# Optimization experiments

Hardware: AMD Instinct MI355X
Metric: run time of the kernel (lower is better)

The kernel has to match this reference:

```python
import jax, jax.numpy as jnp
import numpy as np

NB, BS, NHID, NINP = 6, 200, 1200, 2400  # num_blocks, block_size, nhid, ninp (=2*nhid)
T, B, NTOK = 32, 32, 16000


def _ln(x, g, b):
    mu = x.mean(-1, keepdims=True)
    v = ((x - mu) ** 2).mean(-1, keepdims=True)
    return (x - mu) / jnp.sqrt(v + 1e-5) * g + b


def _attend(q3, k3, v3, wq, wk, wv, wfc, g, b, nh, dk, dv, residual):
    # q3/k3/v3: (B, L, d_model); multi-head scaled-dot attention across blocks
    Bz, L, _ = q3.shape
    qh = (q3 @ wq).reshape(Bz, L, nh, dk)
    kh = (k3 @ wk).reshape(Bz, L, nh, dk)
    vh = (v3 @ wv).reshape(Bz, L, nh, dv)
    att = jnp.einsum('bqhd,bkhd->bhqk', qh, kh) / float(np.sqrt(dk))
    att = jax.nn.softmax(att, axis=-1)
    out = jnp.einsum('bhqk,bkhd->bqhd', att, vh).reshape(Bz, L, nh * dv)
    out = out @ wfc
    if residual:
        out = out + q3
    return _ln(out, g, b)


def setup_inputs() -> dict:
    key = jax.random.key(0)
    ks = jax.random.split(key, 16)
    rn = lambda i, sh, s: jax.random.normal(ks[i], sh, dtype=jnp.float32) * s
    d = {}
    d['tokens'] = jax.random.randint(ks[0], (T, B), 0, NTOK)
    d['h0'] = jnp.zeros((2, B, NHID), jnp.float32)
    d['c0'] = jnp.zeros((2, B, NHID), jnp.float32)
    d['emb_table'] = jax.random.uniform(ks[1], (NTOK, NINP), jnp.float32, -0.1, 0.1)
    d['Wi'] = rn(2, (NB, 4 * BS, NINP), 0.01)
    d['Wh'] = rn(3, (NB, 4 * BS, BS), 0.05)
    d['bih'] = jnp.zeros((NB, 4 * BS), jnp.float32)
    d['bhh'] = jnp.zeros((NB, 4 * BS), jnp.float32)
    d['mq'] = rn(4, (BS, 64), 0.07)
    d['mk'] = rn(5, (BS, 64), 0.07)
    d['mv'] = rn(6, (BS, 64), 0.07)
    d['mfc'] = rn(7, (64, BS), 0.1)
    d['mg'] = jnp.ones((BS,), jnp.float32)
    d['mb'] = jnp.zeros((BS,), jnp.float32)
    d['lq'] = rn(8, (BS, 1600), 0.07)
    d['lk'] = rn(9, (BS, 1600), 0.07)
    d['lv'] = rn(10, (BS, 1600), 0.07)
    d['lfc'] = rn(11, (1600, 2400), 0.02)
    d['lg'] = jnp.ones((2400,), jnp.float32)
    d['lb'] = jnp.zeros((2400,), jnp.float32)
    d['dec_w'] = jax.random.uniform(ks[12], (NTOK, NHID), jnp.float32, -0.1, 0.1)
    d['dec_b'] = jnp.zeros((NTOK,), jnp.float32)
    return d


def reference(tokens, h0, c0, emb_table, Wi, Wh, bih, bhh, mq, mk, mv, mfc, mg, mb,
              lq, lk, lv, lfc, lg, lb, dec_w, dec_b):
    def block_lstm(x, h, c):
        # block-diagonal LSTMCell: k independent cells, per-block input NINP, hidden BS
        Bz = x.shape[0]
        xb = x.reshape(Bz, NB, -1)
        hb = h.reshape(Bz, NB, BS)
        cb = c.reshape(Bz, NB, BS)
        gt = jnp.einsum('bki,kgi->bkg', xb, Wi) + jnp.einsum('bkh,kgh->bkg', hb, Wh) + bih + bhh
        ii, ff, gg, oo = jnp.split(gt, 4, axis=-1)  # torch LSTMCell gate order i,f,g,o
        cn = jax.nn.sigmoid(ff) * cb + jax.nn.sigmoid(ii) * jnp.tanh(gg)
        hn = jax.nn.sigmoid(oo) * jnp.tanh(cn)
        return hn.reshape(Bz, NHID), cn.reshape(Bz, NHID)

    def self_att(h):
        hb = h.reshape(-1, NB, BS)
        hb = _attend(hb, hb, hb, mq, mk, mv, mfc, mg, mb, 4, 16, 16, True)
        return hb.reshape(-1, NHID)

    emb = emb_table[tokens]  # (T, B, NINP)

    def step0(carry, x):
        h, c = carry
        h, c = block_lstm(jnp.tile(x, (1, NB)), h, c)
        h = self_att(h)
        return (h, c), h

    (hf0, cf0), out = jax.lax.scan(step0, (h0[0], c0[0]), emb)

    def step1(carry, x):
        h, c = carry
        q = h.reshape(-1, NB, BS)
        kv = x.reshape(-1, NB, BS)
        inp = _attend(q, kv, kv, lq, lk, lv, lfc, lg, lb, 8, BS, BS, False)  # (B, NB, 2400)
        h, c = block_lstm(inp.reshape(inp.shape[0], -1), h, c)
        h = self_att(h)
        return (h, c), h

    (hf1, cf1), out = jax.lax.scan(step1, (h0[1], c0[1]), out)

    decoded = out @ dec_w.T + dec_b  # (T, B, NTOK)
    return decoded, jnp.stack([hf0, hf1]), jnp.stack([cf0, cf1])
```

## Files before the change

### kernel.cpp

```cpp
#include <hip/hip_runtime.h>
#include <math.h>

#define NBLK 6
#define BS   200
#define NHID 1200
#define NINP 2400
#define TT   32
#define BZ   32
#define NTOK 16000
#define NG   4800
#define ROWS 1024
#define L1D  1600

__device__ __forceinline__ float sigmoidf_(float x) { return 1.0f / (1.0f + expf(-x)); }

template <bool BT>
__global__ __launch_bounds__(256) void gemm128_kernel(
    const float* __restrict__ A, const float* __restrict__ B,
    const float* __restrict__ bias1, const float* __restrict__ bias2,
    float* __restrict__ C, int M, int N, int K, const int* __restrict__ a_idx)
{
    __shared__ __align__(16) float As[8][132];
    __shared__ __align__(16) float Bs[8][132];
    const int tid = threadIdx.x;
    const int tx = tid & 15, ty = tid >> 4;
    const int n0 = blockIdx.x * 128, m0 = blockIdx.y * 128;

    const int la_r = tid >> 1, la_k = (tid & 1) * 4;
    long arow;
    {
        int row = m0 + la_r;
        arow = a_idx ? (long)a_idx[row] * K : (long)row * K;
    }
    float acc[8][8] = {};

    for (int k0 = 0; k0 < K; k0 += 8) {
        {
            float4 v = *(const float4*)&A[arow + k0 + la_k];
            As[la_k + 0][la_r] = v.x;
            As[la_k + 1][la_r] = v.y;
            As[la_k + 2][la_r] = v.z;
            As[la_k + 3][la_r] = v.w;
        }
        if constexpr (!BT) {
            int kk = tid >> 5, n = (tid & 31) * 4;
            int col = n0 + n;
            float4 v = make_float4(0.f, 0.f, 0.f, 0.f);
            if (col < N) v = *(const float4*)&B[(long)(k0 + kk) * N + col];
            *(float4*)&Bs[kk][n] = v;
        } else {
            int n = tid >> 1, kk0 = (tid & 1) * 4;
            int col = n0 + n;
            float4 v = make_float4(0.f, 0.f, 0.f, 0.f);
            if (col < N) v = *(const float4*)&B[(long)col * K + k0 + kk0];
            Bs[kk0 + 0][n] = v.x;
            Bs[kk0 + 1][n] = v.y;
            Bs[kk0 + 2][n] = v.z;
            Bs[kk0 + 3][n] = v.w;
        }
        __syncthreads();
        #pragma unroll
        for (int kk = 0; kk < 8; kk++) {
            float av[8], bv[8];
            *(float4*)&av[0] = *(const float4*)&As[kk][ty * 4];
            *(float4*)&av[4] = *(const float4*)&As[kk][ty * 4 + 64];
            *(float4*)&bv[0] = *(const float4*)&Bs[kk][tx * 4];
            *(float4*)&bv[4] = *(const float4*)&Bs[kk][tx * 4 + 64];
            #pragma unroll
            for (int i = 0; i < 8; i++)
                #pragma unroll
                for (int j = 0; j < 8; j++) acc[i][j] += av[i] * bv[j];
        }
        __syncthreads();
    }
    #pragma unroll
    for (int i = 0; i < 8; i++) {
        int row = m0 + ty * 4 + (i & 3) + (i >> 2) * 64;
        #pragma unroll
        for (int jg = 0; jg < 2; jg++) {
            int col = n0 + tx * 4 + jg * 64;
            if (col < N) {
                float4 v;
                v.x = acc[i][jg * 4 + 0]; v.y = acc[i][jg * 4 + 1];
                v.z = acc[i][jg * 4 + 2]; v.w = acc[i][jg * 4 + 3];
                if (bias1) {
                    float4 b1 = *(const float4*)&bias1[col];
                    v.x += b1.x; v.y += b1.y; v.z += b1.z; v.w += b1.w;
                }
                if (bias2) {
                    float4 b2 = *(const float4*)&bias2[col];
                    v.x += b2.x; v.y += b2.y; v.z += b2.z; v.w += b2.w;
                }
                *(float4*)&C[(long)row * N + col] = v;
            }
        }
    }
}

__global__ __launch_bounds__(256) void gemm_skp_kernel(
    const float* __restrict__ A, const float* __restrict__ B,
    float* __restrict__ Cp, int M, int N, int K, int KL)
{
    __shared__ __align__(16) float As[8][68];
    __shared__ __align__(16) float Bs[8][68];
    const int tid = threadIdx.x;
    const int tx = tid & 15, ty = tid >> 4;
    const int n0 = blockIdx.x * 64, m0 = blockIdx.y * 64;
    const int z = blockIdx.z;
    const int kbeg = z * KL, kend = kbeg + KL;

    float acc[4][4] = {};

    for (int k0 = kbeg; k0 < kend; k0 += 8) {
        {
            int idx = tid * 2;
            int mm = idx >> 3, kk = idx & 7;
            int row = m0 + mm;
            float2 v = *(const float2*)&A[(long)row * K + k0 + kk];
            As[kk][mm] = v.x;
            As[kk + 1][mm] = v.y;
        }
        {
            int idx = tid * 2;
            int nn = idx & 63, kk = idx >> 6;
            int n = n0 + nn;
            float2 v = make_float2(0.f, 0.f);
            if (n < N) v = *(const float2*)&B[(long)(k0 + kk) * N + n];
            Bs[kk][nn] = v.x;
            Bs[kk][nn + 1] = v.y;
        }
        __syncthreads();
        #pragma unroll
        for (int kk = 0; kk < 8; kk++) {
            const float4 a4 = *(const float4*)&As[kk][ty * 4];
            const float4 b4 = *(const float4*)&Bs[kk][tx * 4];
            const float av[4] = {a4.x, a4.y, a4.z, a4.w};
            const float bv[4] = {b4.x, b4.y, b4.z, b4.w};
            #pragma unroll
            for (int i = 0; i < 4; i++)
                #pragma unroll
                for (int j = 0; j < 4; j++) acc[i][j] += av[i] * bv[j];
        }
        __syncthreads();
    }
    float* Cz = Cp + (long)z * M * N;
    #pragma unroll
    for (int i = 0; i < 4; i++) {
        int row = m0 + ty * 4 + i;
        #pragma unroll
        for (int j = 0; j < 4; j++) {
            int col = n0 + tx * 4 + j;
            if (col < N) Cz[(long)row * N + col] = acc[i][j];
        }
    }
}

__global__ __launch_bounds__(256) void bigb_kernel(
    const float* __restrict__ lq, const float* __restrict__ lk,
    float* __restrict__ BigB)
{
    int id = blockIdx.x * 256 + threadIdx.x;
    if (id >= 320000) return;
    int h = id / 40000, r = id % 40000, cp = r / 200, c = r % 200;
    const float4* a = (const float4*)(lq + (long)c * L1D + h * 200);
    const float4* b = (const float4*)(lk + (long)cp * L1D + h * 200);
    float s0 = 0, s1 = 0, s2 = 0, s3 = 0;
    #pragma unroll 5
    for (int d = 0; d < 50; d++) {
        float4 av = a[d], bv = b[d];
        s0 += av.x * bv.x; s1 += av.y * bv.y; s2 += av.z * bv.z; s3 += av.w * bv.w;
    }
    BigB[(long)cp * L1D + h * 200 + c] = s0 + s1 + s2 + s3;
}

__global__ __launch_bounds__(256) void lstm0_kernel(
    const float* __restrict__ GX,
    const float* __restrict__ hprev,
    float* __restrict__ c_io,
    const float* __restrict__ Wh,
    float* __restrict__ h_out)
{
    __shared__ float h_s[200 * 33];
    const int k = blockIdx.y, jt = blockIdx.x, tid = threadIdx.x;
    for (int idx = tid; idx < 1600; idx += 256) {
        int bb = idx / 50, m4 = idx % 50;
        float4 v = *(const float4*)&hprev[bb * NHID + k * BS + m4 * 4];
        h_s[(m4 * 4 + 0) * 33 + bb] = v.x;
        h_s[(m4 * 4 + 1) * 33 + bb] = v.y;
        h_s[(m4 * 4 + 2) * 33 + bb] = v.z;
        h_s[(m4 * 4 + 3) * 33 + bb] = v.w;
    }
    __syncthreads();
    const int b = tid & 31, jj = tid >> 5;
    const int j = jt * 8 + jj;
    const float* w0 = Wh + (long)(k * 800 + j) * 200;
    const float* w1 = w0 + 200 * 200;
    const float* w2 = w0 + 400 * 200;
    const float* w3 = w0 + 600 * 200;
    float a0 = 0, a1 = 0, a2 = 0, a3 = 0;
    for (int m = 0; m < 200; m += 4) {
        float4 wv0 = *(const float4*)&w0[m];
        float4 wv1 = *(const float4*)&w1[m];
        float4 wv2 = *(const float4*)&w2[m];
        float4 wv3 = *(const float4*)&w3[m];
        float h0v = h_s[(m + 0) * 33 + b];
        float h1v = h_s[(m + 1) * 33 + b];
        float h2v = h_s[(m + 2) * 33 + b];
        float h3v = h_s[(m + 3) * 33 + b];
        a0 += h0v * wv0.x + h1v * wv0.y + h2v * wv0.z + h3v * wv0.w;
        a1 += h0v * wv1.x + h1v * wv1.y + h2v * wv1.z + h3v * wv1.w;
        a2 += h0v * wv2.x + h1v * wv2.y + h2v * wv2.z + h3v * wv2.w;
        a3 += h0v * wv3.x + h1v * wv3.y + h2v * wv3.z + h3v * wv3.w;
    }
    const float* gx = GX + b * NG + k * 800;
    float gi = a0 + gx[j];
    float gf = a1 + gx[200 + j];
    float gg = a2 + gx[400 + j];
    float go = a3 + gx[600 + j];
    int o = b * NHID + k * BS + j;
    float cold = c_io[o];
    float cn = sigmoidf_(gf) * cold + sigmoidf_(gi) * tanhf(gg);
    float hn = sigmoidf_(go) * tanhf(cn);
    c_io[o] = cn;
    h_out[o] = hn;
}

__global__ __launch_bounds__(512) void lstm1_kernel(
    const float* __restrict__ inp, const float* __restrict__ hprev,
    float* __restrict__ c_io, const float* __restrict__ Wi,
    const float* __restrict__ Wh, const float* __restrict__ bih,
    const float* __restrict__ bhh, float* __restrict__ h_out)
{
    __shared__ float h_s[200 * 33];
    __shared__ float x_s[2][100 * 33];
    __shared__ float ps[12][128];
    const int k = blockIdx.y, jt = blockIdx.x, tid = threadIdx.x;
    const int b = tid & 31, jg = (tid >> 5) & 3, kh = tid >> 7;
    const int j = jt * 4 + jg;

    for (int idx = tid; idx < 1600; idx += 512) {
        int bb = idx / 50, m4 = idx % 50;
        float4 v = *(const float4*)&hprev[bb * NHID + k * BS + m4 * 4];
        h_s[(m4 * 4 + 0) * 33 + bb] = v.x;
        h_s[(m4 * 4 + 1) * 33 + bb] = v.y;
        h_s[(m4 * 4 + 2) * 33 + bb] = v.z;
        h_s[(m4 * 4 + 3) * 33 + bb] = v.w;
    }
    for (int idx = tid; idx < 800; idx += 512) {
        int bb = idx / 25, m4 = idx % 25;
        float4 v = *(const float4*)&inp[(long)(bb * 6 + k) * NINP + m4 * 4];
        x_s[0][(m4 * 4 + 0) * 33 + bb] = v.x;
        x_s[0][(m4 * 4 + 1) * 33 + bb] = v.y;
        x_s[0][(m4 * 4 + 2) * 33 + bb] = v.z;
        x_s[0][(m4 * 4 + 3) * 33 + bb] = v.w;
    }

    const float* wi0 = Wi + (long)(k * 800 + j) * NINP;
    const float* wi1 = wi0 + (long)200 * NINP;
    const float* wi2 = wi0 + (long)400 * NINP;
    const float* wi3 = wi0 + (long)600 * NINP;
    float a0 = 0, a1 = 0, a2 = 0, a3 = 0;
    int cur = 0;
    for (int ti = 0; ti < 24; ti++) {
        __syncthreads();
        if (ti + 1 < 24) {
            int kt = (ti + 1) * 100;
            float* xs = x_s[cur ^ 1];
            for (int idx = tid; idx < 800; idx += 512) {
                int bb = idx / 25, m4 = idx % 25;
                float4 v = *(const float4*)&inp[(long)(bb * 6 + k) * NINP + kt + m4 * 4];
                xs[(m4 * 4 + 0) * 33 + bb] = v.x;
                xs[(m4 * 4 + 1) * 33 + bb] = v.y;
                xs[(m4 * 4 + 2) * 33 + bb] = v.z;
                xs[(m4 * 4 + 3) * 33 + bb] = v.w;
            }
        }
        if (ti / 6 == kh) {
            const int kt = ti * 100;
            const float* xs = x_s[cur];
            for (int m = 0; m < 100; m += 4) {
                float4 w0 = *(const float4*)&wi0[kt + m];
                float4 w1 = *(const float4*)&wi1[kt + m];
                float4 w2 = *(const float4*)&wi2[kt + m];
                float4 w3 = *(const float4*)&wi3[kt + m];
                float x0 = xs[(m + 0) * 33 + b];
                float x1 = xs[(m + 1) * 33 + b];
                float x2 = xs[(m + 2) * 33 + b];
                float x3 = xs[(m + 3) * 33 + b];
                a0 += x0 * w0.x + x1 * w0.y + x2 * w0.z + x3 * w0.w;
                a1 += x0 * w1.x + x1 * w1.y + x2 * w1.z + x3 * w1.w;
                a2 += x0 * w2.x + x1 * w2.y + x2 * w2.z + x3 * w2.w;
                a3 += x0 * w3.x + x1 * w3.y + x2 * w3.z + x3 * w3.w;
            }
        }
        cur ^= 1;
    }
    if (kh == 0) {
        const float* w0 = Wh + (long)(k * 800 + j) * 200;
        const float* w1 = w0 + 200 * 200;
        const float* w2 = w0 + 400 * 200;
        const float* w3 = w0 + 600 * 200;
        for (int m = 0; m < 200; m += 4) {
            float4 wv0 = *(const float4*)&w0[m];
            float4 wv1 = *(const float4*)&w1[m];
            float4 wv2 = *(const float4*)&w2[m];
            float4 wv3 = *(const float4*)&w3[m];
            float h0v = h_s[(m + 0) * 33 + b];
            float h1v = h_s[(m + 1) * 33 + b];
            float h2v = h_s[(m + 2) * 33 + b];
            float h3v = h_s[(m + 3) * 33 + b];
            a0 += h0v * wv0.x + h1v * wv0.y + h2v * wv0.z + h3v * wv0.w;
            a1 += h0v * wv1.x + h1v * wv1.y + h2v * wv1.z + h3v * wv1.w;
            a2 += h0v * wv2.x + h1v * wv2.y + h2v * wv2.z + h3v * wv2.w;
            a3 += h0v * wv3.x + h1v * wv3.y + h2v * wv3.z + h3v * wv3.w;
        }
    } else {
        int g = (kh - 1) * 4, t = tid & 127;
        ps[g + 0][t] = a0; ps[g + 1][t] = a1; ps[g + 2][t] = a2; ps[g + 3][t] = a3;
    }
    __syncthreads();
    if (kh == 0) {
        a0 += ps[0][tid] + ps[4][tid] + ps[8][tid];
        a1 += ps[1][tid] + ps[5][tid] + ps[9][tid];
        a2 += ps[2][tid] + ps[6][tid] + ps[10][tid];
        a3 += ps[3][tid] + ps[7][tid] + ps[11][tid];
        int nb = k * 800;
        float gi = a0 + bih[nb + j] + bhh[nb + j];
        float gf = a1 + bih[nb + 200 + j] + bhh[nb + 200 + j];
        float gg = a2 + bih[nb + 400 + j] + bhh[nb + 400 + j];
        float go = a3 + bih[nb + 600 + j] + bhh[nb + 600 + j];
        int o = b * NHID + k * BS + j;
        float cold = c_io[o];
        float cn = sigmoidf_(gf) * cold + sigmoidf_(gi) * tanhf(gg);
        float hn = sigmoidf_(go) * tanhf(cn);
        c_io[o] = cn;
        h_out[o] = hn;
    }
}

__global__ __launch_bounds__(256) void att_small_kernel(
    const float* __restrict__ h_in, float* __restrict__ h_out,
    const float* __restrict__ mq, const float* __restrict__ mk,
    const float* __restrict__ mv, const float* __restrict__ mfc,
    const float* __restrict__ mg, const float* __restrict__ mb)
{
    __shared__ float hb[1200];
    __shared__ float qh[384], kh[384], vh[384];
    __shared__ float att[144];
    __shared__ float outp[384];
    __shared__ float o2[1200];
    __shared__ float mu_s[6], rs_s[6];
    const int b = blockIdx.x, tid = threadIdx.x;
    for (int i = tid; i < 300; i += 256)
        ((float4*)hb)[i] = ((const float4*)(h_in + b * NHID))[i];
    __syncthreads();
    if (tid < 192) {
        int which = tid >> 6, hd = tid & 63;
        const float* Mw = which == 0 ? mq : (which == 1 ? mk : mv);
        float acc[6] = {};
        for (int jx = 0; jx < 200; jx++) {
            float w = Mw[jx * 64 + hd];
            #pragma unroll
            for (int l = 0; l < 6; l++) acc[l] += hb[l * 200 + jx] * w;
        }
        float* dst = which == 0 ? qh : (which == 1 ? kh : vh);
        #pragma unroll
        for (int l = 0; l < 6; l++) dst[l * 64 + hd] = acc[l];
    }
    __syncthreads();
    if (tid < 144) {
        int h = tid / 36, r = tid % 36, q = r / 6, kk = r % 6;
        float s = 0;
        #pragma unroll
        for (int d = 0; d < 16; d++) s += qh[q * 64 + h * 16 + d] * kh[kk * 64 + h * 16 + d];
        att[(h * 6 + q) * 6 + kk] = s * 0.25f;
    }
    __syncthreads();
    if (tid < 24) {
        float* a = &att[tid * 6];
        float mx = a[0];
        for (int i = 1; i < 6; i++) mx = fmaxf(mx, a[i]);
        float sm = 0;
        for (int i = 0; i < 6; i++) { a[i] = expf(a[i] - mx); sm += a[i]; }
        float inv = 1.f / sm;
        for (int i = 0; i < 6; i++) a[i] *= inv;
    }
    __syncthreads();
    for (int id = tid; id < 384; id += 256) {
        int q = id >> 6, hd = id & 63, h = hd >> 4;
        float s = 0;
        #pragma unroll
        for (int kk = 0; kk < 6; kk++) s += att[(h * 6 + q) * 6 + kk] * vh[kk * 64 + hd];
        outp[id] = s;
    }
    __syncthreads();
    if (tid < 200) {
        float acc[6] = {};
        for (int d = 0; d < 64; d++) {
            float w = mfc[d * 200 + tid];
            #pragma unroll
            for (int q = 0; q < 6; q++) acc[q] += outp[q * 64 + d] * w;
        }
        #pragma unroll
        for (int q = 0; q < 6; q++) o2[q * 200 + tid] = acc[q] + hb[q * 200 + tid];
    }
    __syncthreads();
    if (tid < 6) {
        const float4* o4 = (const float4*)(o2 + tid * 200);
        float s = 0, s2 = 0;
        for (int i = 0; i < 50; i++) {
            float4 v = o4[i];
            s += v.x + v.y + v.z + v.w;
            s2 += v.x * v.x + v.y * v.y + v.z * v.z + v.w * v.w;
        }
        float mu = s / 200.f;
        float var = s2 / 200.f - mu * mu;
        mu_s[tid] = mu;
        rs_s[tid] = 1.0f / sqrtf(var + 1e-5f);
    }
    __syncthreads();
    for (int i = tid; i < 300; i += 256) {
        int q = i / 50;
        float4 v = ((float4*)o2)[i];
        float4 g4 = ((const float4*)mg)[i % 50];
        float4 b4 = ((const float4*)mb)[i % 50];
        float mu = mu_s[q], rstd = rs_s[q];
        float4 r;
        r.x = (v.x - mu) * rstd * g4.x + b4.x;
        r.y = (v.y - mu) * rstd * g4.y + b4.y;
        r.z = (v.z - mu) * rstd * g4.z + b4.z;
        r.w = (v.w - mu) * rstd * g4.w + b4.w;
        ((float4*)(h_out + b * NHID))[i] = r;
    }
}

__global__ __launch_bounds__(256) void att1_kernel(
    const float* __restrict__ hp,
    const float* __restrict__ KM,
    const float* __restrict__ VH,
    float* __restrict__ attV)
{
    __shared__ float att[288];
    const int b = blockIdx.x, tid = threadIdx.x;
    const float* qb = hp + b * NHID;
    const float* kb = KM + b * 9600;
    const float* vb = VH + b * 9600;
    for (int id = tid; id < 288; id += 256) {
        int h = id / 36, r = id % 36, q = r / 6, kk = r % 6;
        const float4* qr = (const float4*)(qb + q * 200);
        const float4* kr = (const float4*)(kb + kk * L1D + h * 200);
        float s0 = 0, s1 = 0, s2 = 0, s3 = 0;
        #pragma unroll 5
        for (int d = 0; d < 50; d++) {
            float4 a = qr[d], v = kr[d];
            s0 += a.x * v.x; s1 += a.y * v.y; s2 += a.z * v.z; s3 += a.w * v.w;
        }
        att[(h * 6 + q) * 6 + kk] = (s0 + s1 + s2 + s3) * 0.07071067811865475f;
    }
    __syncthreads();
    if (tid < 48) {
        float* a = &att[tid * 6];
        float mx = a[0];
        for (int i = 1; i < 6; i++) mx = fmaxf(mx, a[i]);
        float sm = 0;
        for (int i = 0; i < 6; i++) { a[i] = expf(a[i] - mx); sm += a[i]; }
        float inv = 1.f / sm;
        for (int i = 0; i < 6; i++) a[i] *= inv;
    }
    __syncthreads();
    for (int hd = tid; hd < L1D; hd += 256) {
        int h = hd / 200;
        float v0 = vb[0 * L1D + hd], v1 = vb[1 * L1D + hd], v2 = vb[2 * L1D + hd];
        float v3 = vb[3 * L1D + hd], v4 = vb[4 * L1D + hd], v5 = vb[5 * L1D + hd];
        #pragma unroll
        for (int q = 0; q < 6; q++) {
            const float* a = &att[(h * 6 + q) * 6];
            float s = a[0] * v0 + a[1] * v1 + a[2] * v2 + a[3] * v3 + a[4] * v4 + a[5] * v5;
            attV[b * 9600 + q * L1D + hd] = s;
        }
    }
}

__global__ __launch_bounds__(256) void ln_sum4_kernel(
    const float* __restrict__ Fp, float* __restrict__ Y,
    const float* __restrict__ g, const float* __restrict__ bta)
{
    __shared__ float rowbuf[2400];
    __shared__ float aw[4], bw[4];
    const int r = blockIdx.x, tid = threadIdx.x;
    const long SL = (long)192 * NINP / 4;
    const float4* f0 = (const float4*)(Fp) + (long)r * (NINP / 4);
    float s = 0, s2 = 0;
    for (int i = tid; i < 600; i += 256) {
        float4 a = f0[i], b2 = f0[SL + i], c = f0[2 * SL + i], d = f0[3 * SL + i];
        float4 v;
        v.x = a.x + b2.x + c.x + d.x;
        v.y = a.y + b2.y + c.y + d.y;
        v.z = a.z + b2.z + c.z + d.z;
        v.w = a.w + b2.w + c.w + d.w;
        ((float4*)rowbuf)[i] = v;
        s += v.x + v.y + v.z + v.w;
        s2 += v.x * v.x + v.y * v.y + v.z * v.z + v.w * v.w;
    }
    for (int off = 32; off; off >>= 1) { s += __shfl_down(s, off); s2 += __shfl_down(s2, off); }
    int wid = tid >> 6, lane = tid & 63;
    if (lane == 0) { aw[wid] = s; bw[wid] = s2; }
    __syncthreads();
    if (tid == 0) {
        float a = 0, a2 = 0;
        for (int w = 0; w < 4; w++) { a += aw[w]; a2 += bw[w]; }
        float mu = a / NINP;
        float var = a2 / NINP - mu * mu;
        aw[0] = mu;
        bw[0] = 1.0f / sqrtf(var + 1e-5f);
    }
    __syncthreads();
    float mu = aw[0], rstd = bw[0];
    for (int i = tid; i < 600; i += 256) {
        float4 v = ((float4*)rowbuf)[i];
        float4 g4 = ((const float4*)g)[i];
        float4 b4 = ((const float4*)bta)[i];
        float4 o;
        o.x = (v.x - mu) * rstd * g4.x + b4.x;
        o.y = (v.y - mu) * rstd * g4.y + b4.y;
        o.z = (v.z - mu) * rstd * g4.z + b4.z;
        o.w = (v.w - mu) * rstd * g4.w + b4.w;
        ((float4*)(Y + (long)r * NINP))[i] = o;
    }
}

extern "C" void kernel_launch(void* const* d_in, const int* in_sizes, int n_in,
                              void* d_out, int out_size, void* d_ws, size_t ws_size,
                              hipStream_t stream)
{
    const int*   tokens = (const int*)  d_in[0];
    const float* h0     = (const float*)d_in[1];
    const float* c0     = (const float*)d_in[2];
    const float* emb    = (const float*)d_in[3];
    const float* Wi     = (const float*)d_in[4];
    const float* Wh     = (const float*)d_in[5];
    const float* bih    = (const float*)d_in[6];
    const float* bhh    = (const float*)d_in[7];
    const float* mq     = (const float*)d_in[8];
    const float* mk     = (const float*)d_in[9];
    const float* mv     = (const float*)d_in[10];
    const float* mfc    = (const float*)d_in[11];
    const float* mg     = (const float*)d_in[12];
    const float* mb     = (const float*)d_in[13];
    const float* lq     = (const float*)d_in[14];
    const float* lk     = (const float*)d_in[15];
    const float* lv     = (const float*)d_in[16];
    const float* lfc    = (const float*)d_in[17];
    const float* lg     = (const float*)d_in[18];
    const float* lb     = (const float*)d_in[19];
    const float* dec_w  = (const float*)d_in[20];
    const float* dec_b  = (const float*)d_in[21];
    float* out = (float*)d_out;

    float* p = (float*)d_ws;
    float* GX0  = p; p += (long)ROWS * NG;
    float* out0 = p; p += (long)ROWS * NHID;
    float* out1 = p; p += (long)ROWS * NHID;
    float* KM   = p; p += (long)ROWS * 6 * L1D;
    float* VH1  = p; p += (long)ROWS * 6 * L1D;
    float* attV = p; p += 192 * L1D;
    float* FCp  = p; p += (long)4 * 192 * NINP;
    float* inp  = p; p += 192 * NINP;
    float* htmp = p; p += BZ * NHID;
    float* cb0  = p; p += BZ * NHID;
    float* cb1  = p; p += BZ * NHID;
    float* BigB = p; p += 200 * L1D;

    const int ST = BZ * NHID;

    hipMemcpyAsync(cb0, c0,      ST * sizeof(float), hipMemcpyDeviceToDevice, stream);
    hipMemcpyAsync(cb1, c0 + ST, ST * sizeof(float), hipMemcpyDeviceToDevice, stream);

    bigb_kernel<<<1250, 256, 0, stream>>>(lq, lk, BigB);

    gemm128_kernel<true><<<dim3(NG / 128 + 1, ROWS / 128), 256, 0, stream>>>(
        emb, Wi, bih, bhh, GX0, ROWS, NG, NINP, tokens);

    for (int t = 0; t < TT; t++) {
        const float* hp = (t == 0) ? h0 : out0 + (t - 1) * ST;
        lstm0_kernel<<<dim3(25, 6), 256, 0, stream>>>(
            GX0 + (long)t * BZ * NG, hp, cb0, Wh, htmp);
        att_small_kernel<<<BZ, 256, 0, stream>>>(htmp, out0 + t * ST, mq, mk, mv, mfc, mg, mb);
    }

    gemm128_kernel<false><<<dim3((L1D + 127) / 128, (ROWS * 6) / 128), 256, 0, stream>>>(
        out0, BigB, nullptr, nullptr, KM, ROWS * 6, L1D, BS, nullptr);
    gemm128_kernel<false><<<dim3((L1D + 127) / 128, (ROWS * 6) / 128), 256, 0, stream>>>(
        out0, lv, nullptr, nullptr, VH1, ROWS * 6, L1D, BS, nullptr);

    for (int t = 0; t < TT; t++) {
        const float* hp = (t == 0) ? h0 + ST : out1 + (t - 1) * ST;
        att1_kernel<<<BZ, 256, 0, stream>>>(
            hp, KM + (long)t * BZ * 6 * L1D, VH1 + (long)t * BZ * 6 * L1D, attV);
        gemm_skp_kernel<<<dim3((NINP + 63) / 64, 3, 4), 256, 0, stream>>>(
            attV, lfc, FCp, 192, NINP, L1D, 400);
        ln_sum4_kernel<<<192, 256, 0, stream>>>(FCp, inp, lg, lb);
        lstm1_kernel<<<dim3(50, 6), 512, 0, stream>>>(inp, hp, cb1, Wi, Wh, bih, bhh, htmp);
        att_small_kernel<<<BZ, 256, 0, stream>>>(htmp, out1 + t * ST, mq, mk, mv, mfc, mg, mb);
    }

    gemm128_kernel<true><<<dim3(NTOK / 128, ROWS / 128), 256, 0, stream>>>(
        out1, dec_w, dec_b, nullptr, out, ROWS, NTOK, NHID, nullptr);

    long off = (long)ROWS * NTOK;
    hipMemcpyAsync(out + off,          out0 + 31 * ST, ST * sizeof(float), hipMemcpyDeviceToDevice, stream);
    hipMemcpyAsync(out + off + ST,     out1 + 31 * ST, ST * sizeof(float), hipMemcpyDeviceToDevice, stream);
    hipMemcpyAsync(out + off + 2 * ST, cb0,            ST * sizeof(float), hipMemcpyDeviceToDevice, stream);
    hipMemcpyAsync(out + off + 3 * ST, cb1,            ST * sizeof(float), hipMemcpyDeviceToDevice, stream);
}
```

Before: 10.40 ms.

## Fuse layer-0 recurrence into one persistent kernel and fuse attention stages

```diff
diff --git a/kernel.cpp b/kernel.cpp
--- a/kernel.cpp
+++ b/kernel.cpp
@@ -11,6 +11,7 @@
 #define NG   4800
 #define ROWS 1024
 #define L1D  1600
+#define ST   (BZ*NHID)
 
 __device__ __forceinline__ float sigmoidf_(float x) { return 1.0f / (1.0f + expf(-x)); }
 
@@ -173,56 +174,298 @@
     BigB[(long)cp * L1D + h * 200 + c] = s0 + s1 + s2 + s3;
 }
 
-__global__ __launch_bounds__(256) void lstm0_kernel(
-    const float* __restrict__ GX,
-    const float* __restrict__ hprev,
-    float* __restrict__ c_io,
-    const float* __restrict__ Wh,
-    float* __restrict__ h_out)
-{
-    __shared__ float h_s[200 * 33];
-    const int k = blockIdx.y, jt = blockIdx.x, tid = threadIdx.x;
-    for (int idx = tid; idx < 1600; idx += 256) {
-        int bb = idx / 50, m4 = idx % 50;
-        float4 v = *(const float4*)&hprev[bb * NHID + k * BS + m4 * 4];
-        h_s[(m4 * 4 + 0) * 33 + bb] = v.x;
-        h_s[(m4 * 4 + 1) * 33 + bb] = v.y;
-        h_s[(m4 * 4 + 2) * 33 + bb] = v.z;
-        h_s[(m4 * 4 + 3) * 33 + bb] = v.w;
-    }
-    __syncthreads();
-    const int b = tid & 31, jj = tid >> 5;
-    const int j = jt * 8 + jj;
-    const float* w0 = Wh + (long)(k * 800 + j) * 200;
-    const float* w1 = w0 + 200 * 200;
-    const float* w2 = w0 + 400 * 200;
-    const float* w3 = w0 + 600 * 200;
-    float a0 = 0, a1 = 0, a2 = 0, a3 = 0;
-    for (int m = 0; m < 200; m += 4) {
-        float4 wv0 = *(const float4*)&w0[m];
-        float4 wv1 = *(const float4*)&w1[m];
-        float4 wv2 = *(const float4*)&w2[m];
-        float4 wv3 = *(const float4*)&w3[m];
-        float h0v = h_s[(m + 0) * 33 + b];
-        float h1v = h_s[(m + 1) * 33 + b];
-        float h2v = h_s[(m + 2) * 33 + b];
-        float h3v = h_s[(m + 3) * 33 + b];
-        a0 += h0v * wv0.x + h1v * wv0.y + h2v * wv0.z + h3v * wv0.w;
-        a1 += h0v * wv1.x + h1v * wv1.y + h2v * wv1.z + h3v * wv1.w;
-        a2 += h0v * wv2.x + h1v * wv2.y + h2v * wv2.z + h3v * wv2.w;
-        a3 += h0v * wv3.x + h1v * wv3.y + h2v * wv3.z + h3v * wv3.w;
-    }
-    const float* gx = GX + b * NG + k * 800;
-    float gi = a0 + gx[j];
-    float gf = a1 + gx[200 + j];
-    float gg = a2 + gx[400 + j];
-    float go = a3 + gx[600 + j];
-    int o = b * NHID + k * BS + j;
-    float cold = c_io[o];
-    float cn = sigmoidf_(gf) * cold + sigmoidf_(gi) * tanhf(gg);
-    float hn = sigmoidf_(go) * tanhf(cn);
-    c_io[o] = cn;
-    h_out[o] = hn;
+__global__ __launch_bounds__(256) void whT_kernel(
+    const float* __restrict__ Wh, float* __restrict__ WhT)
+{
+    int id = blockIdx.x * 256 + threadIdx.x;
+    if (id >= 960000) return;
+    int k = id / 160000, r = id % 160000, m = r / 800, g = r % 800;
+    WhT[id] = Wh[(long)(k * 800 + g) * 200 + m];
+}
+
+__device__ __forceinline__ void att_inline(
+    float* hb, float* aux, float* gout,
+    const float* __restrict__ mq, const float* __restrict__ mk,
+    const float* __restrict__ mv, const float* __restrict__ mfc,
+    const float* __restrict__ mg, const float* __restrict__ mb)
+{
+    const int tid = threadIdx.x;
+    float* qh   = aux;
+    float* kh   = aux + 384;
+    float* vh   = aux + 768;
+    float* att  = aux + 1152;
+    float* outp = aux + 1296;
+    float* o2   = aux + 1680;
+    float* mu_s = aux + 2880;
+    float* rs_s = aux + 2888;
+    if (tid < 192) {
+        int which = tid >> 6, hd = tid & 63;
+        const float* Mw = which == 0 ? mq : (which == 1 ? mk : mv);
+        float acc[6] = {};
+        for (int jx = 0; jx < 200; jx++) {
+            float w = Mw[jx * 64 + hd];
+            #pragma unroll
+            for (int l = 0; l < 6; l++) acc[l] += hb[l * 200 + jx] * w;
+        }
+        float* dst = which == 0 ? qh : (which == 1 ? kh : vh);
+        #pragma unroll
+        for (int l = 0; l < 6; l++) dst[l * 64 + hd] = acc[l];
+    }
+    __syncthreads();
+    if (tid < 144) {
+        int h = tid / 36, r = tid % 36, q = r / 6, kk = r % 6;
+        float s = 0;
+        #pragma unroll
+        for (int d = 0; d < 16; d++) s += qh[q * 64 + h * 16 + d] * kh[kk * 64 + h * 16 + d];
+        att[(h * 6 + q) * 6 + kk] = s * 0.25f;
+    }
+    __syncthreads();
+    if (tid < 24) {
+        float* a = att + tid * 6;
+        float mx = a[0];
+        for (int i = 1; i < 6; i++) mx = fmaxf(mx, a[i]);
+        float sm = 0;
+        for (int i = 0; i < 6; i++) { a[i] = expf(a[i] - mx); sm += a[i]; }
+        float inv = 1.f / sm;
+        for (int i = 0; i < 6; i++) a[i] *= inv;
+    }
+    __syncthreads();
+    for (int id = tid; id < 384; id += 256) {
+        int q = id >> 6, hd = id & 63, h = hd >> 4;
+        float s = 0;
+        #pragma unroll
+        for (int kk = 0; kk < 6; kk++) s += att[(h * 6 + q) * 6 + kk] * vh[kk * 64 + hd];
+        outp[id] = s;
+    }
+    __syncthreads();
+    if (tid < 200) {
+        float acc[6] = {};
+        for (int d = 0; d < 64; d++) {
+            float w = mfc[d * 200 + tid];
+            #pragma unroll
+            for (int q = 0; q < 6; q++) acc[q] += outp[q * 64 + d] * w;
+        }
+        #pragma unroll
+        for (int q = 0; q < 6; q++) o2[q * 200 + tid] = acc[q] + hb[q * 200 + tid];
+    }
+    __syncthreads();
+    if (tid < 6) {
+        const float4* o4 = (const float4*)(o2 + tid * 200);
+        float s = 0, s2 = 0;
+        for (int i = 0; i < 50; i++) {
+            float4 v = o4[i];
+            s += v.x + v.y + v.z + v.w;
+            s2 += v.x * v.x + v.y * v.y + v.z * v.z + v.w * v.w;
+        }
+        float mu = s / 200.f;
+        float var = s2 / 200.f - mu * mu;
+        mu_s[tid] = mu;
+        rs_s[tid] = 1.0f / sqrtf(var + 1e-5f);
+    }
+    __syncthreads();
+    for (int i = tid; i < 300; i += 256) {
+        int q = i / 50;
+        float4 v = ((float4*)o2)[i];
+        float4 g4 = ((const float4*)mg)[i % 50];
+        float4 b4 = ((const float4*)mb)[i % 50];
+        float mu = mu_s[q], rstd = rs_s[q];
+        float4 r;
+        r.x = (v.x - mu) * rstd * g4.x + b4.x;
+        r.y = (v.y - mu) * rstd * g4.y + b4.y;
+        r.z = (v.z - mu) * rstd * g4.z + b4.z;
+        r.w = (v.w - mu) * rstd * g4.w + b4.w;
+        ((float4*)hb)[i] = r;
+        if (gout) ((float4*)(gout))[i] = r;
+    }
+    __syncthreads();
+}
+
+__global__ __launch_bounds__(256) void phaseA_kernel(
+    const float* __restrict__ GX0, const float* __restrict__ h0,
+    const float* __restrict__ c0, const float* __restrict__ WhT,
+    float* __restrict__ out0, float* __restrict__ cf0,
+    const float* __restrict__ mq, const float* __restrict__ mk,
+    const float* __restrict__ mv, const float* __restrict__ mfc,
+    const float* __restrict__ mg, const float* __restrict__ mb)
+{
+    __shared__ __align__(16) float h_s[1200];
+    __shared__ __align__(16) float c_s[1200];
+    __shared__ __align__(16) float g_s[4800];
+    __shared__ __align__(16) float gx_s[4800];
+    __shared__ __align__(16) float aux[2896];
+    const int b = blockIdx.x, tid = threadIdx.x;
+    for (int i = tid; i < 300; i += 256) {
+        ((float4*)h_s)[i] = ((const float4*)(h0 + b * NHID))[i];
+        ((float4*)c_s)[i] = ((const float4*)(c0 + b * NHID))[i];
+    }
+    __syncthreads();
+    for (int t = 0; t < TT; t++) {
+        const float4* gx4 = (const float4*)(GX0 + ((long)t * BZ + b) * NG);
+        for (int i = tid; i < 1200; i += 256) ((float4*)gx_s)[i] = gx4[i];
+        if (tid < 200) {
+            #pragma unroll
+            for (int k = 0; k < 6; k++) {
+                const float* wp = WhT + (long)k * 160000 + tid * 4;
+                float a0 = 0, a1 = 0, a2 = 0, a3 = 0;
+                for (int m = 0; m < 200; m++) {
+                    float hv = h_s[k * 200 + m];
+                    float4 w = *(const float4*)(wp + (long)m * 800);
+                    a0 += hv * w.x; a1 += hv * w.y; a2 += hv * w.z; a3 += hv * w.w;
+                }
+                int gb = k * 800 + tid * 4;
+                g_s[gb] = a0; g_s[gb + 1] = a1; g_s[gb + 2] = a2; g_s[gb + 3] = a3;
+            }
+        }
+        __syncthreads();
+        for (int idx = tid; idx < 1200; idx += 256) {
+            int k = idx / 200, j = idx - k * 200;
+            int base = k * 800 + j;
+            float gi = g_s[base] + gx_s[base];
+            float gf = g_s[base + 200] + gx_s[base + 200];
+            float gg = g_s[base + 400] + gx_s[base + 400];
+            float go = g_s[base + 600] + gx_s[base + 600];
+            float cn = sigmoidf_(gf) * c_s[idx] + sigmoidf_(gi) * tanhf(gg);
+            c_s[idx] = cn;
+            h_s[idx] = sigmoidf_(go) * tanhf(cn);
+        }
+        __syncthreads();
+        att_inline(h_s, aux, out0 + (long)t * ST + b * NHID, mq, mk, mv, mfc, mg, mb);
+    }
+    for (int i = tid; i < 300; i += 256)
+        ((float4*)(cf0 + b * NHID))[i] = ((float4*)c_s)[i];
+}
+
+template <bool FIRST>
+__global__ __launch_bounds__(256) void fusedatt_kernel(
+    const float* __restrict__ htmp, const float* __restrict__ h0l1,
+    float* __restrict__ out1_prev,
+    const float* __restrict__ KMt, const float* __restrict__ VHt,
+    float* __restrict__ attV,
+    const float* __restrict__ mq, const float* __restrict__ mk,
+    const float* __restrict__ mv, const float* __restrict__ mfc,
+    const float* __restrict__ mg, const float* __restrict__ mb)
+{
+    __shared__ __align__(16) float hb[1200];
+    __shared__ __align__(16) float aux[2896];
+    __shared__ float attp[72];
+    __shared__ float attr[36];
+    const int blk = blockIdx.x, b = blk >> 3, h = blk & 7, tid = threadIdx.x;
+    if (FIRST) {
+        for (int i = tid; i < 300; i += 256)
+            ((float4*)hb)[i] = ((const float4*)(h0l1 + b * NHID))[i];
+        __syncthreads();
+    } else {
+        for (int i = tid; i < 300; i += 256)
+            ((float4*)hb)[i] = ((const float4*)(htmp + b * NHID))[i];
+        __syncthreads();
+        att_inline(hb, aux, (h == 0) ? out1_prev + b * NHID : nullptr,
+                   mq, mk, mv, mfc, mg, mb);
+    }
+    const float* kb = KMt + (long)b * 9600 + h * 200;
+    if (tid < 72) {
+        int r = tid >> 1, half = tid & 1;
+        int q = r / 6, kk = r % 6;
+        const float4* qr = (const float4*)(hb + q * 200 + half * 100);
+        const float4* kr = (const float4*)(kb + (long)kk * L1D + half * 100);
+        float s0 = 0, s1 = 0, s2 = 0, s3 = 0;
+        #pragma unroll 5
+        for (int d = 0; d < 25; d++) {
+            float4 a = qr[d], v = kr[d];
+            s0 += a.x * v.x; s1 += a.y * v.y; s2 += a.z * v.z; s3 += a.w * v.w;
+        }
+        attp[tid] = s0 + s1 + s2 + s3;
+    }
+    __syncthreads();
+    if (tid < 6) {
+        float v[6]; float mx = -1e30f;
+        #pragma unroll
+        for (int kk = 0; kk < 6; kk++) {
+            float s = (attp[(tid * 6 + kk) * 2] + attp[(tid * 6 + kk) * 2 + 1]) * 0.07071067811865475f;
+            v[kk] = s; mx = fmaxf(mx, s);
+        }
+        float sm = 0;
+        #pragma unroll
+        for (int kk = 0; kk < 6; kk++) { v[kk] = expf(v[kk] - mx); sm += v[kk]; }
+        float inv = 1.f / sm;
+        #pragma unroll
+        for (int kk = 0; kk < 6; kk++) attr[tid * 6 + kk] = v[kk] * inv;
+    }
+    __syncthreads();
+    if (tid < 200) {
+        int hd = h * 200 + tid;
+        const float* vb = VHt + (long)b * 9600 + hd;
+        float v0 = vb[0], v1 = vb[L1D], v2 = vb[2 * L1D];
+        float v3 = vb[3 * L1D], v4 = vb[4 * L1D], v5 = vb[5 * L1D];
+        #pragma unroll
+        for (int q = 0; q < 6; q++) {
+            const float* a = attr + q * 6;
+            attV[(long)b * 9600 + q * L1D + hd] =
+                a[0] * v0 + a[1] * v1 + a[2] * v2 + a[3] * v3 + a[4] * v4 + a[5] * v5;
+        }
+    }
+}
+
+__global__ __launch_bounds__(256) void attsmall_kernel(
+    const float* __restrict__ h_in, float* __restrict__ h_out,
+    const float* __restrict__ mq, const float* __restrict__ mk,
+    const float* __restrict__ mv, const float* __restrict__ mfc,
+    const float* __restrict__ mg, const float* __restrict__ mb)
+{
+    __shared__ __align__(16) float hb[1200];
+    __shared__ __align__(16) float aux[2896];
+    const int b = blockIdx.x, tid = threadIdx.x;
+    for (int i = tid; i < 300; i += 256)
+        ((float4*)hb)[i] = ((const float4*)(h_in + b * NHID))[i];
+    __syncthreads();
+    att_inline(hb, aux, h_out + b * NHID, mq, mk, mv, mfc, mg, mb);
+}
+
+__global__ __launch_bounds__(256) void ln_sum8_kernel(
+    const float* __restrict__ Fp, float* __restrict__ Y,
+    const float* __restrict__ g, const float* __restrict__ bta)
+{
+    __shared__ float rowbuf[2400];
+    __shared__ float aw[4], bw[4];
+    const int r = blockIdx.x, tid = threadIdx.x;
+    const long SL = (long)192 * NINP / 4;
+    const float4* f0 = (const float4*)(Fp) + (long)r * (NINP / 4);
+    float s = 0, s2 = 0;
+    for (int i = tid; i < 600; i += 256) {
+        float4 v = f0[i];
+        #pragma unroll
+        for (int z = 1; z < 8; z++) {
+            float4 a = f0[(long)z * SL + i];
+            v.x += a.x; v.y += a.y; v.z += a.z; v.w += a.w;
+        }
+        ((float4*)rowbuf)[i] = v;
+        s += v.x + v.y + v.z + v.w;
+        s2 += v.x * v.x + v.y * v.y + v.z * v.z + v.w * v.w;
+    }
+    for (int off = 32; off; off >>= 1) { s += __shfl_down(s, off); s2 += __shfl_down(s2, off); }
+    int wid = tid >> 6, lane = tid & 63;
+    if (lane == 0) { aw[wid] = s; bw[wid] = s2; }
+    __syncthreads();
+    if (tid == 0) {
+        float a = 0, a2 = 0;
+        for (int w = 0; w < 4; w++) { a += aw[w]; a2 += bw[w]; }
+        float mu = a / NINP;
+        float var = a2 / NINP - mu * mu;
+        aw[0] = mu;
+        bw[0] = 1.0f / sqrtf(var + 1e-5f);
+    }
+    __syncthreads();
+    float mu = aw[0], rstd = bw[0];
+    for (int i = tid; i < 600; i += 256) {
+        float4 v = ((float4*)rowbuf)[i];
+        float4 g4 = ((const float4*)g)[i];
+        float4 b4 = ((const float4*)bta)[i];
+        float4 o;
+        o.x = (v.x - mu) * rstd * g4.x + b4.x;
+        o.y = (v.y - mu) * rstd * g4.y + b4.y;
+        o.z = (v.z - mu) * rstd * g4.z + b4.z;
+        o.w = (v.w - mu) * rstd * g4.w + b4.w;
+        ((float4*)(Y + (long)r * NINP))[i] = o;
+    }
 }
 
 __global__ __launch_bounds__(512) void lstm1_kernel(
@@ -283,10 +526,8 @@
                 float4 w1 = *(const float4*)&wi1[kt + m];
                 float4 w2 = *(const float4*)&wi2[kt + m];
                 float4 w3 = *(const float4*)&wi3[kt + m];
-                float x0 = xs[(m + 0) * 33 + b];
-                float x1 = xs[(m + 1) * 33 + b];
-                float x2 = xs[(m + 2) * 33 + b];
-                float x3 = xs[(m + 3) * 33 + b];
+                float x0 = xs[(m + 0) * 33 + b], x1 = xs[(m + 1) * 33 + b];
+                float x2 = xs[(m + 2) * 33 + b], x3 = xs[(m + 3) * 33 + b];
                 a0 += x0 * w0.x + x1 * w0.y + x2 * w0.z + x3 * w0.w;
                 a1 += x0 * w1.x + x1 * w1.y + x2 * w1.z + x3 * w1.w;
                 a2 += x0 * w2.x + x1 * w2.y + x2 * w2.z + x3 * w2.w;
@@ -305,18 +546,16 @@
             float4 wv1 = *(const float4*)&w1[m];
             float4 wv2 = *(const float4*)&w2[m];
             float4 wv3 = *(const float4*)&w3[m];
-            float h0v = h_s[(m + 0) * 33 + b];
-            float h1v = h_s[(m + 1) * 33 + b];
-            float h2v = h_s[(m + 2) * 33 + b];
-            float h3v = h_s[(m + 3) * 33 + b];
+            float h0v = h_s[(m + 0) * 33 + b], h1v = h_s[(m + 1) * 33 + b];
+            float h2v = h_s[(m + 2) * 33 + b], h3v = h_s[(m + 3) * 33 + b];
             a0 += h0v * wv0.x + h1v * wv0.y + h2v * wv0.z + h3v * wv0.w;
             a1 += h0v * wv1.x + h1v * wv1.y + h2v * wv1.z + h3v * wv1.w;
             a2 += h0v * wv2.x + h1v * wv2.y + h2v * wv2.z + h3v * wv2.w;
             a3 += h0v * wv3.x + h1v * wv3.y + h2v * wv3.z + h3v * wv3.w;
         }
     } else {
-        int g = (kh - 1) * 4, t = tid & 127;
-        ps[g + 0][t] = a0; ps[g + 1][t] = a1; ps[g + 2][t] = a2; ps[g + 3][t] = a3;
+        int g = (kh - 1) * 4, t2 = tid & 127;
+        ps[g + 0][t2] = a0; ps[g + 1][t2] = a1; ps[g + 2][t2] = a2; ps[g + 3][t2] = a3;
     }
     __syncthreads();
     if (kh == 0) {
@@ -324,208 +563,17 @@
         a1 += ps[1][tid] + ps[5][tid] + ps[9][tid];
         a2 += ps[2][tid] + ps[6][tid] + ps[10][tid];
         a3 += ps[3][tid] + ps[7][tid] + ps[11][tid];
-        int nb = k * 800;
-        float gi = a0 + bih[nb + j] + bhh[nb + j];
-        float gf = a1 + bih[nb + 200 + j] + bhh[nb + 200 + j];
-        float gg = a2 + bih[nb + 400 + j] + bhh[nb + 400 + j];
-        float go = a3 + bih[nb + 600 + j] + bhh[nb + 600 + j];
+        int nb2 = k * 800;
+        float gi = a0 + bih[nb2 + j] + bhh[nb2 + j];
+        float gf = a1 + bih[nb2 + 200 + j] + bhh[nb2 + 200 + j];
+        float gg = a2 + bih[nb2 + 400 + j] + bhh[nb2 + 400 + j];
+        float go = a3 + bih[nb2 + 600 + j] + bhh[nb2 + 600 + j];
         int o = b * NHID + k * BS + j;
         float cold = c_io[o];
         float cn = sigmoidf_(gf) * cold + sigmoidf_(gi) * tanhf(gg);
         float hn = sigmoidf_(go) * tanhf(cn);
         c_io[o] = cn;
         h_out[o] = hn;
-    }
-}
-
-__global__ __launch_bounds__(256) void att_small_kernel(
-    const float* __restrict__ h_in, float* __restrict__ h_out,
-    const float* __restrict__ mq, const float* __restrict__ mk,
-    const float* __restrict__ mv, const float* __restrict__ mfc,
-    const float* __restrict__ mg, const float* __restrict__ mb)
-{
-    __shared__ float hb[1200];
-    __shared__ float qh[384], kh[384], vh[384];
-    __shared__ float att[144];
-    __shared__ float outp[384];
-    __shared__ float o2[1200];
-    __shared__ float mu_s[6], rs_s[6];
-    const int b = blockIdx.x, tid = threadIdx.x;
-    for (int i = tid; i < 300; i += 256)
-        ((float4*)hb)[i] = ((const float4*)(h_in + b * NHID))[i];
-    __syncthreads();
-    if (tid < 192) {
-        int which = tid >> 6, hd = tid & 63;
-        const float* Mw = which == 0 ? mq : (which == 1 ? mk : mv);
-        float acc[6] = {};
-        for (int jx = 0; jx < 200; jx++) {
-            float w = Mw[jx * 64 + hd];
-            #pragma unroll
-            for (int l = 0; l < 6; l++) acc[l] += hb[l * 200 + jx] * w;
-        }
-        float* dst = which == 0 ? qh : (which == 1 ? kh : vh);
-        #pragma unroll
-        for (int l = 0; l < 6; l++) dst[l * 64 + hd] = acc[l];
-    }
-    __syncthreads();
-    if (tid < 144) {
-        int h = tid / 36, r = tid % 36, q = r / 6, kk = r % 6;
-        float s = 0;
-        #pragma unroll
-        for (int d = 0; d < 16; d++) s += qh[q * 64 + h * 16 + d] * kh[kk * 64 + h * 16 + d];
-        att[(h * 6 + q) * 6 + kk] = s * 0.25f;
-    }
-    __syncthreads();
-    if (tid < 24) {
-        float* a = &att[tid * 6];
-        float mx = a[0];
-        for (int i = 1; i < 6; i++) mx = fmaxf(mx, a[i]);
-        float sm = 0;
-        for (int i = 0; i < 6; i++) { a[i] = expf(a[i] - mx); sm += a[i]; }
-        float inv = 1.f / sm;
-        for (int i = 0; i < 6; i++) a[i] *= inv;
-    }
-    __syncthreads();
-    for (int id = tid; id < 384; id += 256) {
-        int q = id >> 6, hd = id & 63, h = hd >> 4;
-        float s = 0;
-        #pragma unroll
-        for (int kk = 0; kk < 6; kk++) s += att[(h * 6 + q) * 6 + kk] * vh[kk * 64 + hd];
-        outp[id] = s;
-    }
-    __syncthreads();
-    if (tid < 200) {
-        float acc[6] = {};
-        for (int d = 0; d < 64; d++) {
-            float w = mfc[d * 200 + tid];
-            #pragma unroll
-            for (int q = 0; q < 6; q++) acc[q] += outp[q * 64 + d] * w;
-        }
-        #pragma unroll
-        for (int q = 0; q < 6; q++) o2[q * 200 + tid] = acc[q] + hb[q * 200 + tid];
-    }
-    __syncthreads();
-    if (tid < 6) {
-        const float4* o4 = (const float4*)(o2 + tid * 200);
-        float s = 0, s2 = 0;
-        for (int i = 0; i < 50; i++) {
-            float4 v = o4[i];
-            s += v.x + v.y + v.z + v.w;
-            s2 += v.x * v.x + v.y * v.y + v.z * v.z + v.w * v.w;
-        }
-        float mu = s / 200.f;
-        float var = s2 / 200.f - mu * mu;
-        mu_s[tid] = mu;
-        rs_s[tid] = 1.0f / sqrtf(var + 1e-5f);
-    }
-    __syncthreads();
-    for (int i = tid; i < 300; i += 256) {
-        int q = i / 50;
-        float4 v = ((float4*)o2)[i];
-        float4 g4 = ((const float4*)mg)[i % 50];
-        float4 b4 = ((const float4*)mb)[i % 50];
-        float mu = mu_s[q], rstd = rs_s[q];
-        float4 r;
-        r.x = (v.x - mu) * rstd * g4.x + b4.x;
-        r.y = (v.y - mu) * rstd * g4.y + b4.y;
-        r.z = (v.z - mu) * rstd * g4.z + b4.z;
-        r.w = (v.w - mu) * rstd * g4.w + b4.w;
-        ((float4*)(h_out + b * NHID))[i] = r;
-    }
-}
-
-__global__ __launch_bounds__(256) void att1_kernel(
-    const float* __restrict__ hp,
-    const float* __restrict__ KM,
-    const float* __restrict__ VH,
-    float* __restrict__ attV)
-{
-    __shared__ float att[288];
-    const int b = blockIdx.x, tid = threadIdx.x;
-    const float* qb = hp + b * NHID;
-    const float* kb = KM + b * 9600;
-    const float* vb = VH + b * 9600;
-    for (int id = tid; id < 288; id += 256) {
-        int h = id / 36, r = id % 36, q = r / 6, kk = r % 6;
-        const float4* qr = (const float4*)(qb + q * 200);
-        const float4* kr = (const float4*)(kb + kk * L1D + h * 200);
-        float s0 = 0, s1 = 0, s2 = 0, s3 = 0;
-        #pragma unroll 5
-        for (int d = 0; d < 50; d++) {
-            float4 a = qr[d], v = kr[d];
-            s0 += a.x * v.x; s1 += a.y * v.y; s2 += a.z * v.z; s3 += a.w * v.w;
-        }
-        att[(h * 6 + q) * 6 + kk] = (s0 + s1 + s2 + s3) * 0.07071067811865475f;
-    }
-    __syncthreads();
-    if (tid < 48) {
-        float* a = &att[tid * 6];
-        float mx = a[0];
-        for (int i = 1; i < 6; i++) mx = fmaxf(mx, a[i]);
-        float sm = 0;
-        for (int i = 0; i < 6; i++) { a[i] = expf(a[i] - mx); sm += a[i]; }
-        float inv = 1.f / sm;
-        for (int i = 0; i < 6; i++) a[i] *= inv;
-    }
-    __syncthreads();
-    for (int hd = tid; hd < L1D; hd += 256) {
-        int h = hd / 200;
-        float v0 = vb[0 * L1D + hd], v1 = vb[1 * L1D + hd], v2 = vb[2 * L1D + hd];
-        float v3 = vb[3 * L1D + hd], v4 = vb[4 * L1D + hd], v5 = vb[5 * L1D + hd];
-        #pragma unroll
-        for (int q = 0; q < 6; q++) {
-            const float* a = &att[(h * 6 + q) * 6];
-            float s = a[0] * v0 + a[1] * v1 + a[2] * v2 + a[3] * v3 + a[4] * v4 + a[5] * v5;
-            attV[b * 9600 + q * L1D + hd] = s;
-        }
-    }
-}
-
-__global__ __launch_bounds__(256) void ln_sum4_kernel(
-    const float* __restrict__ Fp, float* __restrict__ Y,
-    const float* __restrict__ g, const float* __restrict__ bta)
-{
-    __shared__ float rowbuf[2400];
-    __shared__ float aw[4], bw[4];
-    const int r = blockIdx.x, tid = threadIdx.x;
-    const long SL = (long)192 * NINP / 4;
-    const float4* f0 = (const float4*)(Fp) + (long)r * (NINP / 4);
-    float s = 0, s2 = 0;
-    for (int i = tid; i < 600; i += 256) {
-        float4 a = f0[i], b2 = f0[SL + i], c = f0[2 * SL + i], d = f0[3 * SL + i];
-        float4 v;
-        v.x = a.x + b2.x + c.x + d.x;
-        v.y = a.y + b2.y + c.y + d.y;
-        v.z = a.z + b2.z + c.z + d.z;
-        v.w = a.w + b2.w + c.w + d.w;
-        ((float4*)rowbuf)[i] = v;
-        s += v.x + v.y + v.z + v.w;
-        s2 += v.x * v.x + v.y * v.y + v.z * v.z + v.w * v.w;
-    }
-    for (int off = 32; off; off >>= 1) { s += __shfl_down(s, off); s2 += __shfl_down(s2, off); }
-    int wid = tid >> 6, lane = tid & 63;
-    if (lane == 0) { aw[wid] = s; bw[wid] = s2; }
-    __syncthreads();
-    if (tid == 0) {
-        float a = 0, a2 = 0;
-        for (int w = 0; w < 4; w++) { a += aw[w]; a2 += bw[w]; }
-        float mu = a / NINP;
-        float var = a2 / NINP - mu * mu;
-        aw[0] = mu;
-        bw[0] = 1.0f / sqrtf(var + 1e-5f);
-    }
-    __syncthreads();
-    float mu = aw[0], rstd = bw[0];
-    for (int i = tid; i < 600; i += 256) {
-        float4 v = ((float4*)rowbuf)[i];
-        float4 g4 = ((const float4*)g)[i];
-        float4 b4 = ((const float4*)bta)[i];
-        float4 o;
-        o.x = (v.x - mu) * rstd * g4.x + b4.x;
-        o.y = (v.y - mu) * rstd * g4.y + b4.y;
-        o.z = (v.z - mu) * rstd * g4.z + b4.z;
-        o.w = (v.w - mu) * rstd * g4.w + b4.w;
-        ((float4*)(Y + (long)r * NINP))[i] = o;
     }
 }
 
@@ -564,29 +612,26 @@
     float* KM   = p; p += (long)ROWS * 6 * L1D;
     float* VH1  = p; p += (long)ROWS * 6 * L1D;
     float* attV = p; p += 192 * L1D;
-    float* FCp  = p; p += (long)4 * 192 * NINP;
+    float* FCp  = p; p += (long)8 * 192 * NINP;
     float* inp  = p; p += 192 * NINP;
     float* htmp = p; p += BZ * NHID;
-    float* cb0  = p; p += BZ * NHID;
     float* cb1  = p; p += BZ * NHID;
     float* BigB = p; p += 200 * L1D;
-
-    const int ST = BZ * NHID;
-
-    hipMemcpyAsync(cb0, c0,      ST * sizeof(float), hipMemcpyDeviceToDevice, stream);
+    float* WhT  = p; p += 6 * 200 * 800;
+
+    long off = (long)ROWS * NTOK;
+    float* cf0 = out + off + 2 * ST;
+
     hipMemcpyAsync(cb1, c0 + ST, ST * sizeof(float), hipMemcpyDeviceToDevice, stream);
 
     bigb_kernel<<<1250, 256, 0, stream>>>(lq, lk, BigB);
+    whT_kernel<<<3750, 256, 0, stream>>>(Wh, WhT);
 
     gemm128_kernel<true><<<dim3(NG / 128 + 1, ROWS / 128), 256, 0, stream>>>(
         emb, Wi, bih, bhh, GX0, ROWS, NG, NINP, tokens);
 
-    for (int t = 0; t < TT; t++) {
-        const float* hp = (t == 0) ? h0 : out0 + (t - 1) * ST;
-        lstm0_kernel<<<dim3(25, 6), 256, 0, stream>>>(
-            GX0 + (long)t * BZ * NG, hp, cb0, Wh, htmp);
-        att_small_kernel<<<BZ, 256, 0, stream>>>(htmp, out0 + t * ST, mq, mk, mv, mfc, mg, mb);
-    }
+    phaseA_kernel<<<BZ, 256, 0, stream>>>(
+        GX0, h0, c0, WhT, out0, cf0, mq, mk, mv, mfc, mg, mb);
 
     gemm128_kernel<false><<<dim3((L1D + 127) / 128, (ROWS * 6) / 128), 256, 0, stream>>>(
         out0, BigB, nullptr, nullptr, KM, ROWS * 6, L1D, BS, nullptr);
@@ -594,22 +639,28 @@
         out0, lv, nullptr, nullptr, VH1, ROWS * 6, L1D, BS, nullptr);
 
     for (int t = 0; t < TT; t++) {
-        const float* hp = (t == 0) ? h0 + ST : out1 + (t - 1) * ST;
-        att1_kernel<<<BZ, 256, 0, stream>>>(
-            hp, KM + (long)t * BZ * 6 * L1D, VH1 + (long)t * BZ * 6 * L1D, attV);
-        gemm_skp_kernel<<<dim3((NINP + 63) / 64, 3, 4), 256, 0, stream>>>(
-            attV, lfc, FCp, 192, NINP, L1D, 400);
-        ln_sum4_kernel<<<192, 256, 0, stream>>>(FCp, inp, lg, lb);
+        const float* hp = (t == 0) ? h0 + ST : out1 + (long)(t - 1) * ST;
+        const float* KMt = KM + (long)t * BZ * 6 * L1D;
+        const float* VHt = VH1 + (long)t * BZ * 6 * L1D;
+        if (t == 0) {
+            fusedatt_kernel<true><<<256, 256, 0, stream>>>(
+                nullptr, h0 + ST, nullptr, KMt, VHt, attV, mq, mk, mv, mfc, mg, mb);
+        } else {
+            fusedatt_kernel<false><<<256, 256, 0, stream>>>(
+                htmp, nullptr, out1 + (long)(t - 1) * ST, KMt, VHt, attV,
+                mq, mk, mv, mfc, mg, mb);
+        }
+        gemm_skp_kernel<<<dim3((NINP + 63) / 64, 3, 8), 256, 0, stream>>>(
+            attV, lfc, FCp, 192, NINP, L1D, 200);
+        ln_sum8_kernel<<<192, 256, 0, stream>>>(FCp, inp, lg, lb);
         lstm1_kernel<<<dim3(50, 6), 512, 0, stream>>>(inp, hp, cb1, Wi, Wh, bih, bhh, htmp);
-        att_small_kernel<<<BZ, 256, 0, stream>>>(htmp, out1 + t * ST, mq, mk, mv, mfc, mg, mb);
-    }
+    }
+    attsmall_kernel<<<BZ, 256, 0, stream>>>(htmp, out1 + (long)31 * ST, mq, mk, mv, mfc, mg, mb);
 
     gemm128_kernel<true><<<dim3(NTOK / 128, ROWS / 128), 256, 0, stream>>>(
         out1, dec_w, dec_b, nullptr, out, ROWS, NTOK, NHID, nullptr);
 
-    long off = (long)ROWS * NTOK;
-    hipMemcpyAsync(out + off,          out0 + 31 * ST, ST * sizeof(float), hipMemcpyDeviceToDevice, stream);
-    hipMemcpyAsync(out + off + ST,     out1 + 31 * ST, ST * sizeof(float), hipMemcpyDeviceToDevice, stream);
-    hipMemcpyAsync(out + off + 2 * ST, cb0,            ST * sizeof(float), hipMemcpyDeviceToDevice, stream);
-    hipMemcpyAsync(out + off + 3 * ST, cb1,            ST * sizeof(float), hipMemcpyDeviceToDevice, stream);
-}
+    hipMemcpyAsync(out + off,          out0 + (long)31 * ST, ST * sizeof(float), hipMemcpyDeviceToDevice, stream);
+    hipMemcpyAsync(out + off + ST,     out1 + (long)31 * ST, ST * sizeof(float), hipMemcpyDeviceToDevice, stream);
+    hipMemcpyAsync(out + off + 3 * ST, cb1,                  ST * sizeof(float), hipMemcpyDeviceToDevice, stream);
+}
```

Result: slower. 10.64 ms (+2.3%).
